# Kernel optimization log

Measured on AMD Instinct MI355X. Metric: run time of the kernel, lower is better.

The kernel has to match this reference:

```python
import jax, jax.numpy as jnp
import numpy as np
import math

D_MODEL = 1024
D_STATE = 16
D_CONV = 4
EXPAND = 2
D_INNER = EXPAND * D_MODEL
DT_RANK = 64
BATCH = 4
SEQ_LEN = 2048


def setup_inputs() -> dict:
    key = jax.random.key(0)
    ks = jax.random.split(key, 10)
    hidden_states = jax.random.normal(ks[0], (BATCH, SEQ_LEN, D_MODEL), jnp.float32)
    in_proj_w = jax.random.normal(ks[1], (D_MODEL, 2 * D_INNER), jnp.float32) * (D_MODEL ** -0.5)
    conv_w = jax.random.normal(ks[2], (D_INNER, D_CONV), jnp.float32) * (D_CONV ** -0.5)
    conv_b = jnp.zeros((D_INNER,), jnp.float32)
    x_proj_w = jax.random.normal(ks[3], (D_INNER, DT_RANK + 2 * D_STATE), jnp.float32) * (D_INNER ** -0.5)
    dt_init_std = DT_RANK ** -0.5
    dt_proj_w = jax.random.uniform(ks[4], (DT_RANK, D_INNER), jnp.float32, -dt_init_std, dt_init_std)
    # inverse-softplus init of dt bias: dt ~ logUniform(dt_min, dt_max)
    dt_min, dt_max, dt_floor = 0.001, 0.1, 1e-4
    dt = jnp.exp(jax.random.uniform(ks[5], (D_INNER,), jnp.float32) * (math.log(dt_max) - math.log(dt_min)) + math.log(dt_min))
    dt = jnp.clip(dt, dt_floor, None)
    dt_proj_b = dt + jnp.log(-jnp.expm1(-dt))
    A = jnp.tile(jnp.arange(1, D_STATE + 1, dtype=jnp.float32)[None, :], (D_INNER, 1))
    A_log = jnp.log(A)
    D = jnp.ones((D_INNER,), jnp.float32)
    out_proj_w = jax.random.normal(ks[6], (D_INNER, D_MODEL), jnp.float32) * (D_INNER ** -0.5)
    return {
        "hidden_states": hidden_states,
        "in_proj_w": in_proj_w,
        "conv_w": conv_w,
        "conv_b": conv_b,
        "x_proj_w": x_proj_w,
        "dt_proj_w": dt_proj_w,
        "dt_proj_b": dt_proj_b,
        "A_log": A_log,
        "D": D,
        "out_proj_w": out_proj_w,
    }


def _mamba_forward(hidden_states, in_proj_w, conv_w, conv_b, x_proj_w, dt_proj_w, dt_proj_b, A_log, D, out_proj_w):
    b, L, _ = hidden_states.shape
    d_state = A_log.shape[1]
    dt_rank = dt_proj_w.shape[0]
    K = conv_w.shape[1]

    xz = hidden_states @ in_proj_w                     # (b, L, 2*d_inner)
    x, z = jnp.split(xz, 2, axis=-1)                   # each (b, L, d_inner)

    # causal depthwise conv1d (padding = K-1, truncated to L)
    x_pad = jnp.pad(x, ((0, 0), (K - 1, 0), (0, 0)))
    x = sum(x_pad[:, k:k + L, :] * conv_w[:, k] for k in range(K)) + conv_b
    x = jax.nn.silu(x)

    x_dbl = x @ x_proj_w                               # (b, L, dt_rank + 2*d_state)
    dt, B, C = jnp.split(x_dbl, [dt_rank, dt_rank + d_state], axis=-1)
    dt = jax.nn.softplus(dt @ dt_proj_w + dt_proj_b)   # (b, L, d_inner)
    A = -jnp.exp(A_log)                                # (d_inner, d_state)

    def step(h, inp):
        x_t, dt_t, B_t, C_t = inp                      # (b,d), (b,d), (b,n), (b,n)
        dA = jnp.exp(A[None] * dt_t[..., None])        # (b, d, n)
        h = dA * h + dt_t[..., None] * B_t[:, None, :] * x_t[..., None]
        y_t = jnp.einsum('bdn,bn->bd', h, C_t) + D * x_t
        return h, y_t

    h0 = jnp.zeros((b, x.shape[-1], d_state), x.dtype)
    xs = (x.transpose(1, 0, 2), dt.transpose(1, 0, 2), B.transpose(1, 0, 2), C.transpose(1, 0, 2))
    _, ys = jax.lax.scan(step, h0, xs)                 # ys: (L, b, d_inner)
    y = ys.transpose(1, 0, 2) * jax.nn.silu(z)
    return y @ out_proj_w                              # (b, L, d_model)


def reference(hidden_states, in_proj_w, conv_w, conv_b, x_proj_w, dt_proj_w, dt_proj_b, A_log, D, out_proj_w):
    return _mamba_forward(hidden_states, in_proj_w, conv_w, conv_b, x_proj_w, dt_proj_w, dt_proj_b, A_log, D, out_proj_w)
```

## Files before the change

### kernel.cpp

```cpp
#include <hip/hip_runtime.h>
#include <hip/hip_bf16.h>


#define DM 1024
#define DS 16
#define DC 4
#define DI 2048
#define DR 64
#define NB 4
#define SL 2048
#define NTOK (NB*SL)
#define XDBL_W (DR + 2*DS)
#define CONV_R 8

typedef __hip_bfloat16 bf16;
typedef unsigned short u16;
typedef __attribute__((ext_vector_type(8))) short s8v;
typedef __attribute__((ext_vector_type(4))) float f4v;
typedef __attribute__((ext_vector_type(4))) unsigned short us4;

__device__ __forceinline__ float b2f(bf16 v) { return __bfloat162float(v); }
__device__ __forceinline__ bf16  f2b(float v) { return __float2bfloat16(v); }
__device__ __forceinline__ u16 f2u(float x) {
    union { bf16 h; u16 s; } u; u.h = f2b(x); return u.s;
}
__device__ __forceinline__ float u2f(u16 s) {
    union { bf16 h; u16 s; } u; u.s = s; return b2f(u.h);
}

__device__ __forceinline__ bool sniff_bf16(const void* Dones) {
    return ((const u16*)Dones)[0] == 0x3F80u;
}

__device__ __forceinline__ float softplus_fast(float v) {
    return fmaxf(v, 0.f) + __logf(1.f + __expf(-fabsf(v)));
}

template<int MODE>
__device__ __forceinline__ float ld(const void* p, size_t i, bool bf) {
    if (MODE == 0) return b2f(((const bf16*)p)[i]);
    if (MODE == 1) return ((const float*)p)[i];
    return bf ? b2f(((const bf16*)p)[i]) : ((const float*)p)[i];
}
template<int MODE>
__device__ __forceinline__ void st(void* p, size_t i, bool bf, float v) {
    if (MODE == 0)      { ((bf16*)p)[i] = f2b(v); }
    else if (MODE == 1) { ((float*)p)[i] = v; }
    else { if (bf) ((bf16*)p)[i] = f2b(v); else ((float*)p)[i] = v; }
}

template<int CM>
__device__ __forceinline__ void cstore(void* C, void* C2, size_t m, int n,
                                       int ldc, bool bf, float v) {
    if (CM == 3) {
        if (n < DR) ((bf16*)C2)[m * DR + n] = f2b(v);
        else        ((float*)C)[m * (2 * DS) + (n - DR)] = v;
    } else {
        st<CM>(C, m * (size_t)ldc + n, bf, v);
    }
}

#define AS1 __attribute__((address_space(1)))
#define AS3 __attribute__((address_space(3)))
__device__ __forceinline__ void gload_lds16(const void* g, void* l) {
    __builtin_amdgcn_global_load_lds((const AS1 unsigned int*)g,
                                     (AS3 unsigned int*)l, 16, 0, 0);
}

__global__ __launch_bounds__(256) void cast_bf16_kernel(
    const void* __restrict__ src, bf16* __restrict__ dst,
    const void* __restrict__ sniff)
{
    const bool bf = sniff_bf16(sniff);
    const size_t i = ((size_t)blockIdx.x * 256 + threadIdx.x) * 4;
    if (bf) {
        *(us4*)((u16*)dst + i) = *(const us4*)((const u16*)src + i);
    } else {
        const f4v f = *(const f4v*)((const float*)src + i);
        us4 o; o.x = f2u(f.x); o.y = f2u(f.y); o.z = f2u(f.z); o.w = f2u(f.w);
        *(us4*)((u16*)dst + i) = o;
    }
}

__global__ __launch_bounds__(256) void transpose_w(
    const void* __restrict__ w, bf16* __restrict__ wt,
    int K, int N, const void* __restrict__ sniff)
{
    const bool bf = sniff_bf16(sniff);
    __shared__ float t[32][33];
    const int tx = threadIdx.x & 31, ty = threadIdx.x >> 5;
    const int n0 = blockIdx.x * 32, k0 = blockIdx.y * 32;
    #pragma unroll
    for (int i = 0; i < 4; i++) {
        int k = k0 + ty + i * 8, n = n0 + tx;
        t[ty + i * 8][tx] = (n < N) ? ld<2>(w, (size_t)k * N + n, bf) : 0.f;
    }
    __syncthreads();
    #pragma unroll
    for (int i = 0; i < 4; i++) {
        int n = n0 + ty + i * 8, k = k0 + tx;
        wt[(size_t)n * K + k] = f2b(t[tx][ty + i * 8]);
    }
}

template<int BM, int BN, int WM, int WN, int CM>
__global__ __launch_bounds__(WM*WN*64, 2) void gemm_big(
    const bf16* __restrict__ A, int lda,
    const bf16* __restrict__ Bt,
    void* __restrict__ C, int ldc, int K,
    const void* __restrict__ sniff)
{
    constexpr int NT  = WM * WN;
    constexpr int NTH = NT * 64;
    constexpr int WAVE_M = BM / WM, WAVE_N = BN / WN;
    constexpr int MR = WAVE_M / 16, NR = WAVE_N / 16, MR2 = MR / 2;
    constexpr int CH_ROWS = NTH / 8;
    constexpr int ACH = BM / CH_ROWS;
    constexpr int BCH = BN / CH_ROWS;

    const bool bf = sniff_bf16(sniff);
    __shared__ short Asm[2][BM * 64];
    __shared__ short Bsm[2][BN * 64];

    const int tid = threadIdx.x, lane = tid & 63, wave = tid >> 6;
    const int wm = wave / WN, wn = wave % WN;
    const int ll = lane & 15, qd = lane >> 4;
    const int m0 = blockIdx.x * BM, n0 = blockIdx.y * BN;

    const int s_r  = tid >> 3;
    const int s_cb = ((tid & 7) * 16) ^ ((s_r & 7) << 4);

    const char* Ab = (const char*)A;
    const char* Bb = (const char*)Bt;

    f4v acc[MR][NR];
    #pragma unroll
    for (int i = 0; i < MR; i++)
        #pragma unroll
        for (int j = 0; j < NR; j++) acc[i][j] = (f4v){0.f, 0.f, 0.f, 0.f};

    #pragma unroll
    for (int c = 0; c < ACH; c++)
        gload_lds16(Ab + (((size_t)(m0 + c * CH_ROWS + s_r) * lda) << 1) + s_cb,
                    (char*)&Asm[0][0] + (c * NTH + tid) * 16);
    #pragma unroll
    for (int c = 0; c < BCH; c++)
        gload_lds16(Bb + (((size_t)(n0 + c * CH_ROWS + s_r) * K) << 1) + s_cb,
                    (char*)&Bsm[0][0] + (c * NTH + tid) * 16);
    asm volatile("s_waitcnt vmcnt(0)" ::: "memory");
    __builtin_amdgcn_sched_barrier(0);
    __builtin_amdgcn_s_barrier();

    const int NTILE = K >> 6;
    for (int t = 0; t < NTILE; ++t) {
        const int cur = t & 1, nxt = cur ^ 1;
        const int kk = (t + 1) << 6;
        const bool more = (t + 1 < NTILE);
        const char* Ac = (const char*)&Asm[cur][0];
        const char* Bc = (const char*)&Bsm[cur][0];
        #pragma unroll
        for (int p = 0; p < 4; ++p) {
            const int kh = p >> 1, mh = p & 1;
            const int kb = kh * 64;
            s8v af[MR2], bv[NR];
            #pragma unroll
            for (int i = 0; i < MR2; i++) {
                const int row = wm * WAVE_M + (mh * MR2 + i) * 16 + ll;
                af[i] = *(const s8v*)(Ac + (size_t)row * 128
                                        + ((kb + qd * 16) ^ ((ll & 7) << 4)));
            }
            #pragma unroll
            for (int j = 0; j < NR; j++) {
                const int row = wn * WAVE_N + j * 16 + ll;
                bv[j] = *(const s8v*)(Bc + (size_t)row * 128
                                        + ((kb + qd * 16) ^ ((ll & 7) << 4)));
            }
            if (p == 0 && more) {
                #pragma unroll
                for (int c = 0; c < ACH; c++)
                    gload_lds16(Ab + (((size_t)(m0 + c * CH_ROWS + s_r) * lda + kk) << 1) + s_cb,
                                (char*)&Asm[nxt][0] + (c * NTH + tid) * 16);
            }
            if (p == 1 && more) {
                #pragma unroll
                for (int c = 0; c < BCH; c++)
                    gload_lds16(Bb + (((size_t)(n0 + c * CH_ROWS + s_r) * K + kk) << 1) + s_cb,
                                (char*)&Bsm[nxt][0] + (c * NTH + tid) * 16);
            }
            __builtin_amdgcn_sched_barrier(0);
            __builtin_amdgcn_s_barrier();
            asm volatile("s_waitcnt lgkmcnt(0)" ::: "memory");
            __builtin_amdgcn_sched_barrier(0);
            __builtin_amdgcn_s_setprio(1);
            #pragma unroll
            for (int i = 0; i < MR2; i++)
                #pragma unroll
                for (int j = 0; j < NR; j++)
                    acc[mh * MR2 + i][j] = __builtin_amdgcn_mfma_f32_16x16x32_bf16(
                        af[i], bv[j], acc[mh * MR2 + i][j], 0, 0, 0);
            __builtin_amdgcn_s_setprio(0);
            if (p == 3) {
                asm volatile("s_waitcnt vmcnt(0)" ::: "memory");
            }
            __builtin_amdgcn_sched_barrier(0);
            __builtin_amdgcn_s_barrier();
        }
    }

    #pragma unroll
    for (int i = 0; i < MR; i++) {
        #pragma unroll
        for (int j = 0; j < NR; j++) {
            const int col = n0 + wn * WAVE_N + j * 16 + ll;
            #pragma unroll
            for (int r = 0; r < 4; r++) {
                const int row = m0 + wm * WAVE_M + i * 16 + qd * 4 + r;
                st<CM>(C, (size_t)row * ldc + col, bf, acc[i][j][r]);
            }
        }
    }
}

template<int CM, int EPI>
__global__ __launch_bounds__(256) void gemm_mfma(
    const bf16* __restrict__ A, int lda,
    const bf16* __restrict__ Bt,
    void* __restrict__ C, void* __restrict__ C2, int ldc,
    int M, int N, int K,
    const void* __restrict__ bias,
    const void* __restrict__ sniff)
{
    const bool bf = sniff_bf16(sniff);
    __shared__ short As[128 * 32];
    __shared__ short Bs[128 * 32];

    const int tid  = threadIdx.x;
    const int lane = tid & 63;
    const int wave = tid >> 6;
    const int wm = (wave & 1) * 64;
    const int wn = (wave >> 1) * 64;
    const int m0 = blockIdx.x * 128;
    const int n0 = blockIdx.y * 128;
    const int ll = lane & 15;
    const int qd = lane >> 4;

    const int srow  = lane >> 2;
    const int skoff = (lane & 3) * 8;

    const short* Ag = (const short*)A;
    const short* Bg = (const short*)Bt;
    char* AsB = (char*)As + wave * 2048 + lane * 16;
    char* BsB = (char*)Bs + wave * 2048 + lane * 16;
    const size_t a_row = (size_t)(m0 + wave * 32 + srow);
    const size_t b_row = (size_t)(n0 + wave * 32 + srow);

    f4v acc[4][4];
    #pragma unroll
    for (int i = 0; i < 4; i++)
        #pragma unroll
        for (int j = 0; j < 4; j++)
            acc[i][j] = (f4v){0.f, 0.f, 0.f, 0.f};

    for (int k0 = 0; k0 < K; k0 += 32) {
        gload_lds16(Ag + a_row * lda + k0 + skoff,            AsB);
        gload_lds16(Ag + (a_row + 16) * lda + k0 + skoff,     AsB + 1024);
        gload_lds16(Bg + b_row * K + k0 + skoff,              BsB);
        gload_lds16(Bg + (b_row + 16) * K + k0 + skoff,       BsB + 1024);
        __syncthreads();

        s8v af[4], bfr[4];
        #pragma unroll
        for (int s = 0; s < 4; s++)
            af[s] = *(const s8v*)&As[(wm + s * 16 + ll) * 32 + qd * 8];
        #pragma unroll
        for (int s = 0; s < 4; s++)
            bfr[s] = *(const s8v*)&Bs[(wn + s * 16 + ll) * 32 + qd * 8];
        #pragma unroll
        for (int i = 0; i < 4; i++)
            #pragma unroll
            for (int j = 0; j < 4; j++)
                acc[i][j] = __builtin_amdgcn_mfma_f32_16x16x32_bf16(
                    af[i], bfr[j], acc[i][j], 0, 0, 0);
        __syncthreads();
    }

    #pragma unroll
    for (int sn = 0; sn < 4; sn++) {
        const int cn = n0 + wn + sn * 16 + ll;
        if (cn >= N) continue;
        float bvv = 0.f;
        if (EPI == 1) bvv = ld<2>(bias, cn, bf);
        #pragma unroll
        for (int sm = 0; sm < 4; sm++) {
            #pragma unroll
            for (int r = 0; r < 4; r++) {
                const int cm = m0 + wm + sm * 16 + qd * 4 + r;
                float v = acc[sm][sn][r];
                if (EPI == 1) v = softplus_fast(v + bvv);
                cstore<CM>(C, C2, (size_t)cm, cn, ldc, bf, v);
            }
        }
    }
}

template<int AM, int CM, int EPI>
__global__ __launch_bounds__(256) void gemm_kernel(
    const void* __restrict__ A, int lda,
    const void* __restrict__ B, size_t bbase, int ldb,
    void* __restrict__ C, void* __restrict__ C2, int ldc,
    int M, int N, int K,
    const void* __restrict__ bias,
    const void* __restrict__ sniff)
{
    const bool bf = sniff_bf16(sniff);
    const int BM = 64, BN = 64, BK = 16;
    __shared__ float Asm[BK][BM + 4];
    __shared__ float Bsm[BK][BN + 4];

    const int tid = threadIdx.x;
    const int m0 = blockIdx.x * BM;
    const int n0 = blockIdx.y * BN;
    const int tx = tid % 16;
    const int ty = tid / 16;
    const int a_k = tid % BK;
    const int a_m = tid / BK;
    const int b_n = tid % BN;
    const int b_k = tid / BN;

    float acc[4][4] = {};

    for (int k0 = 0; k0 < K; k0 += BK) {
        #pragma unroll
        for (int i = 0; i < 4; i++) {
            int m = m0 + a_m + i * 16;
            float v = 0.f;
            if (m < M) v = ld<AM>(A, (size_t)m * lda + (k0 + a_k), bf);
            Asm[a_k][a_m + i * 16] = v;
        }
        #pragma unroll
        for (int i = 0; i < 4; i++) {
            int kk = b_k + i * 4;
            int n = n0 + b_n;
            float v = 0.f;
            if (n < N) v = ld<2>(B, bbase + (size_t)(k0 + kk) * ldb + n, bf);
            Bsm[kk][b_n] = v;
        }
        __syncthreads();
        #pragma unroll
        for (int kk = 0; kk < BK; kk++) {
            float av[4], bv[4];
            #pragma unroll
            for (int i = 0; i < 4; i++) av[i] = Asm[kk][ty * 4 + i];
            #pragma unroll
            for (int j = 0; j < 4; j++) bv[j] = Bsm[kk][tx * 4 + j];
            #pragma unroll
            for (int i = 0; i < 4; i++)
                #pragma unroll
                for (int j = 0; j < 4; j++)
                    acc[i][j] += av[i] * bv[j];
        }
        __syncthreads();
    }
    #pragma unroll
    for (int i = 0; i < 4; i++) {
        int m = m0 + ty * 4 + i;
        if (m >= M) continue;
        #pragma unroll
        for (int j = 0; j < 4; j++) {
            int n = n0 + tx * 4 + j;
            if (n >= N) continue;
            float v = acc[i][j];
            if (EPI == 1) {
                v += ld<2>(bias, n, bf);
                v = softplus_fast(v);
            }
            cstore<CM>(C, C2, (size_t)m, n, ldc, bf, v);
        }
    }
}

__global__ __launch_bounds__(256) void conv_silu_kernel(
    const bf16* __restrict__ xg, const void* __restrict__ w,
    const void* __restrict__ bias, bf16* __restrict__ xc,
    const void* __restrict__ sniff)
{
    const bool bf = sniff_bf16(sniff);
    const int c  = blockIdx.x * 256 + threadIdx.x;
    const int r0 = blockIdx.y * CONV_R;
    const int l0 = r0 % SL;

    float w0, w1, w2, w3;
    if (bf) {
        const us4 wv = *(const us4*)((const u16*)w + (size_t)c * 4);
        w0 = u2f(wv.x); w1 = u2f(wv.y); w2 = u2f(wv.z); w3 = u2f(wv.w);
    } else {
        const f4v wv = *(const f4v*)((const float*)w + (size_t)c * 4);
        w0 = wv.x; w1 = wv.y; w2 = wv.z; w3 = wv.w;
    }
    const float bs = ld<2>(bias, c, bf);

    float xm3 = (l0 >= 3) ? b2f(xg[(size_t)(r0 - 3) * DI + c]) : 0.f;
    float xm2 = (l0 >= 2) ? b2f(xg[(size_t)(r0 - 2) * DI + c]) : 0.f;
    float xm1 = (l0 >= 1) ? b2f(xg[(size_t)(r0 - 1) * DI + c]) : 0.f;

    #pragma unroll
    for (int i = 0; i < CONV_R; i++) {
        const size_t row = (size_t)(r0 + i);
        const float x0 = b2f(xg[row * DI + c]);
        const float acc = bs + w0 * xm3 + w1 * xm2 + w2 * xm1 + w3 * x0;
        const float s = acc / (1.f + __expf(-acc));
        xc[row * DI + c] = f2b(s);
        xm3 = xm2; xm2 = xm1; xm1 = x0;
    }
}

__global__ __launch_bounds__(256) void scan_pass1(
    const bf16* __restrict__ xc, const bf16* __restrict__ dt,
    const float* __restrict__ bc,
    const void* __restrict__ A_log, const void* __restrict__ Dones,
    float* __restrict__ P, float* __restrict__ Q, int nch)
{
    const bool bf = sniff_bf16(Dones);
    const int d = blockIdx.x * 256 + threadIdx.x;
    const int c = blockIdx.y;
    const int b = blockIdx.z;
    const int T = SL / nch;
    __shared__ float bcs[64 * 2 * DS];

    const size_t base = (size_t)b * SL + (size_t)c * T;
    for (int k = threadIdx.x; k < T * 2 * DS; k += 256)
        bcs[k] = bc[base * (2 * DS) + k];

    float a[DS], Qq[DS];
    bool lad = true;
    #pragma unroll
    for (int n = 0; n < DS; n++) {
        a[n] = -__expf(ld<2>(A_log, (size_t)d * DS + n, bf));
        Qq[n] = 0.f;
        lad = lad && (fabsf(a[n] - (n + 1) * a[0]) < 1e-3f);
    }
    __syncthreads();

    const u16* xp = (const u16*)xc + base * DI + d;
    const u16* tp = (const u16*)dt + base * DI + d;

    float Pp[DS];
    if (lad) {
        const float a0 = a[0];
        float R = 1.f;
        for (int i = 0; i < T; i++) {
            const float xv = u2f(xp[(size_t)i * DI]);
            const float tv = u2f(tp[(size_t)i * DI]);
            const float dtx = tv * xv;
            const float* Bv = &bcs[i * 2 * DS];
            const float r = __expf(a0 * tv);
            const float r2 = r * r, r3 = r2 * r, r4 = r2 * r2;
            float ca = r, cb = r2, cc = r3, cd = r4;
            R *= r;
            #pragma unroll
            for (int n = 0; n < DS; n += 4) {
                Qq[n]     = ca * Qq[n]     + dtx * Bv[n];
                Qq[n + 1] = cb * Qq[n + 1] + dtx * Bv[n + 1];
                Qq[n + 2] = cc * Qq[n + 2] + dtx * Bv[n + 2];
                Qq[n + 3] = cd * Qq[n + 3] + dtx * Bv[n + 3];
                ca *= r4; cb *= r4; cc *= r4; cd *= r4;
            }
        }
        const float R2 = R * R, R3 = R2 * R, R4 = R2 * R2;
        float pa = R, pb = R2, pc = R3, pd = R4;
        #pragma unroll
        for (int n = 0; n < DS; n += 4) {
            Pp[n] = pa; Pp[n + 1] = pb; Pp[n + 2] = pc; Pp[n + 3] = pd;
            pa *= R4; pb *= R4; pc *= R4; pd *= R4;
        }
    } else {
        #pragma unroll
        for (int n = 0; n < DS; n++) Pp[n] = 1.f;
        for (int i = 0; i < T; i++) {
            const float xv = u2f(xp[(size_t)i * DI]);
            const float tv = u2f(tp[(size_t)i * DI]);
            const float dtx = tv * xv;
            const float* Bv = &bcs[i * 2 * DS];
            #pragma unroll
            for (int n = 0; n < DS; n++) {
                const float dA = __expf(a[n] * tv);
                Pp[n] *= dA;
                Qq[n] = dA * Qq[n] + dtx * Bv[n];
            }
        }
    }
    const size_t ob = ((size_t)b * nch + c) * (DS * DI) + d;
    #pragma unroll
    for (int n = 0; n < DS; n++) {
        P[ob + (size_t)n * DI] = Pp[n];
        Q[ob + (size_t)n * DI] = Qq[n];
    }
}

__global__ __launch_bounds__(256) void scan_pass2(
    float* __restrict__ P, const float* __restrict__ Q, int nch)
{
    const int j = blockIdx.x * 256 + threadIdx.x;
    const int b = blockIdx.y;
    float h = 0.f;
    for (int c = 0; c < nch; c++) {
        const size_t o = ((size_t)b * nch + c) * (DI * DS) + j;
        const float p = P[o];
        const float q = Q[o];
        P[o] = h;
        h = p * h + q;
    }
}

__global__ __launch_bounds__(256) void scan_pass3(
    const bf16* __restrict__ xc, const bf16* __restrict__ dt,
    const float* __restrict__ bc, bf16* __restrict__ z,
    const void* __restrict__ A_log, const void* __restrict__ Dones,
    const float* __restrict__ H, int nch)
{
    const bool bf = sniff_bf16(Dones);
    const int d = blockIdx.x * 256 + threadIdx.x;
    const int c = blockIdx.y;
    const int b = blockIdx.z;
    const int T = SL / nch;
    __shared__ float bcs[64 * 2 * DS];

    const size_t base = (size_t)b * SL + (size_t)c * T;
    for (int k = threadIdx.x; k < T * 2 * DS; k += 256)
        bcs[k] = bc[base * (2 * DS) + k];

    float a[DS], h[DS];
    bool lad = true;
    const size_t ob = ((size_t)b * nch + c) * (DS * DI) + d;
    #pragma unroll
    for (int n = 0; n < DS; n++) {
        a[n] = -__expf(ld<2>(A_log, (size_t)d * DS + n, bf));
        h[n] = H[ob + (size_t)n * DI];
        lad = lad && (fabsf(a[n] - (n + 1) * a[0]) < 1e-3f);
    }
    const float dD = ld<2>(Dones, d, bf);
    __syncthreads();

    const u16* xp = (const u16*)xc + base * DI + d;
    const u16* tp = (const u16*)dt + base * DI + d;
    u16*       zp = (u16*)z + base * DI + d;

    if (lad) {
        const float a0 = a[0];
        for (int i = 0; i < T; i++) {
            const float xv = u2f(xp[(size_t)i * DI]);
            const float tv = u2f(tp[(size_t)i * DI]);
            const float zv = u2f(zp[(size_t)i * DI]);
            const float dtx = tv * xv;
            const float* Bv = &bcs[i * 2 * DS];
            const float* Cv = Bv + DS;
            const float r = __expf(a0 * tv);
            const float r2 = r * r, r3 = r2 * r, r4 = r2 * r2;
            float ca = r, cb = r2, cc = r3, cd = r4;
            float ya = dD * xv, yb = 0.f, yc = 0.f, yd = 0.f;
            #pragma unroll
            for (int n = 0; n < DS; n += 4) {
                h[n]     = ca * h[n]     + dtx * Bv[n];     ya += h[n]     * Cv[n];
                h[n + 1] = cb * h[n + 1] + dtx * Bv[n + 1]; yb += h[n + 1] * Cv[n + 1];
                h[n + 2] = cc * h[n + 2] + dtx * Bv[n + 2]; yc += h[n + 2] * Cv[n + 2];
                h[n + 3] = cd * h[n + 3] + dtx * Bv[n + 3]; yd += h[n + 3] * Cv[n + 3];
                ca *= r4; cb *= r4; cc *= r4; cd *= r4;
            }
            const float y = (ya + yb) + (yc + yd);
            const float g = zv / (1.f + __expf(-zv));
            zp[(size_t)i * DI] = f2u(y * g);
        }
    } else {
        for (int i = 0; i < T; i++) {
            const float xv = u2f(xp[(size_t)i * DI]);
            const float tv = u2f(tp[(size_t)i * DI]);
            const float zv = u2f(zp[(size_t)i * DI]);
            const float dtx = tv * xv;
            const float* Bv = &bcs[i * 2 * DS];
            const float* Cv = Bv + DS;
            float y = dD * xv;
            #pragma unroll
            for (int n = 0; n < DS; n++) {
                const float dA = __expf(a[n] * tv);
                h[n] = dA * h[n] + dtx * Bv[n];
                y += h[n] * Cv[n];
            }
            const float g = zv / (1.f + __expf(-zv));
            zp[(size_t)i * DI] = f2u(y * g);
        }
    }
}

__global__ __launch_bounds__(256) void scan_serial(
    const bf16* __restrict__ xc, const bf16* __restrict__ dt,
    const float* __restrict__ bc, bf16* __restrict__ z,
    const void* __restrict__ A_log, const void* __restrict__ Dones)
{
    const bool bf = sniff_bf16(Dones);
    const int d = blockIdx.x * 256 + threadIdx.x;
    const int b = blockIdx.y;
    float a[DS], h[DS];
    #pragma unroll
    for (int n = 0; n < DS; n++) {
        a[n] = -__expf(ld<2>(A_log, (size_t)d * DS + n, bf));
        h[n] = 0.f;
    }
    const float dD = ld<2>(Dones, d, bf);
    const size_t base = (size_t)b * SL;
    for (int l = 0; l < SL; l++) {
        const size_t row = base + l;
        const float xv  = b2f(xc[row * DI + d]);
        const float dtv = b2f(dt[row * DI + d]);
        const float* Bv = bc + row * (2 * DS);
        const float dtx = dtv * xv;
        float y = dD * xv;
        #pragma unroll
        for (int n = 0; n < DS; n++) {
            const float dA = __expf(a[n] * dtv);
            h[n] = dA * h[n] + dtx * Bv[n];
            y += h[n] * Bv[DS + n];
        }
        const float zv = b2f(z[row * DI + d]);
        const float g = zv / (1.f + __expf(-zv));
        z[row * DI + d] = f2b(y * g);
    }
}

extern "C" void kernel_launch(void* const* d_in, const int* in_sizes, int n_in,
                              void* d_out, int out_size, void* d_ws, size_t ws_size,
                              hipStream_t stream) {
    const void* hs        = d_in[0];
    const void* in_proj_w = d_in[1];
    const void* conv_w    = d_in[2];
    const void* conv_b    = d_in[3];
    const void* x_proj_w  = d_in[4];
    const void* dt_proj_w = d_in[5];
    const void* dt_proj_b = d_in[6];
    const void* A_log     = d_in[7];
    const void* Dones     = d_in[8];
    const void* out_proj_w= d_in[9];

    char* ws = (char*)d_ws;
    bf16*  xg   = (bf16*)(ws);
    bf16*  xc   = (bf16*)(ws + 33554432);
    bf16*  hsb  = (bf16*)(ws + 33554432);
    bf16*  z    = (bf16*)(ws + 67108864);
    float* bc   = (float*)(ws + 100663296);
    bf16*  dtf  = (bf16*)(ws + 101711872);
    const size_t WT_OFF = 102760448;
    bf16* in_projT  = (bf16*)(ws + WT_OFF);
    bf16* x_projT   = (bf16*)(ws + WT_OFF);
    bf16* dt_projT  = (bf16*)(ws + WT_OFF + 524288);
    bf16* out_projT = (bf16*)(ws + WT_OFF);
    const bool mfma_ok = ws_size >= WT_OFF + 8388608;

    const size_t per_chunk = (size_t)NB * DI * DS * 4 * 2;
    int nch = 32;
    while (nch > 1 && WT_OFF + (size_t)nch * per_chunk > ws_size) nch >>= 1;
    const bool chunked = (WT_OFF + (size_t)nch * per_chunk <= ws_size);
    float* P = (float*)(ws + WT_OFF);
    float* Q = P + (size_t)NB * nch * DI * DS;

    bf16* dtb = xg;

    if (mfma_ok) {
        cast_bf16_kernel<<<(NTOK*DM/4)/256, 256, 0, stream>>>(hs, hsb, Dones);
        transpose_w<<<dim3((2*DI)/32, DM/32), 256, 0, stream>>>(
            in_proj_w, in_projT, DM, 2*DI, Dones);
        gemm_big<256, 256, 2, 4, 0><<<dim3(NTOK/256, DI/256), 512, 0, stream>>>(
            hsb, DM, in_projT, xg, DI, DM, Dones);
        gemm_big<256, 256, 2, 4, 0><<<dim3(NTOK/256, DI/256), 512, 0, stream>>>(
            hsb, DM, in_projT + (size_t)DI * DM, z, DI, DM, Dones);
        conv_silu_kernel<<<dim3(DI/256, NTOK/CONV_R), 256, 0, stream>>>(
            xg, conv_w, conv_b, xc, Dones);
        transpose_w<<<dim3(128/32, DI/32), 256, 0, stream>>>(
            x_proj_w, x_projT, DI, XDBL_W, Dones);
        gemm_mfma<3, 0><<<dim3(NTOK/128, 1), 256, 0, stream>>>(
            xc, DI, x_projT, bc, dtf, 0, NTOK, XDBL_W, DI, nullptr, Dones);
        transpose_w<<<dim3(DI/32, DR/32), 256, 0, stream>>>(
            dt_proj_w, dt_projT, DR, DI, Dones);
        gemm_mfma<0, 1><<<dim3(NTOK/128, DI/128), 256, 0, stream>>>(
            dtf, DR, dt_projT, dtb, nullptr, DI, NTOK, DI, DR, dt_proj_b, Dones);
    } else {
        gemm_kernel<2, 0, 0><<<dim3(NTOK/64, DI/64), 256, 0, stream>>>(
            hs, DM, in_proj_w, 0, 2*DI, xg, nullptr, DI, NTOK, DI, DM, nullptr, Dones);
        gemm_kernel<2, 0, 0><<<dim3(NTOK/64, DI/64), 256, 0, stream>>>(
            hs, DM, in_proj_w, DI, 2*DI, z, nullptr, DI, NTOK, DI, DM, nullptr, Dones);
        conv_silu_kernel<<<dim3(DI/256, NTOK/CONV_R), 256, 0, stream>>>(
            xg, conv_w, conv_b, xc, Dones);
        gemm_kernel<0, 3, 0><<<dim3(NTOK/64, (XDBL_W + 63)/64), 256, 0, stream>>>(
            xc, DI, x_proj_w, 0, XDBL_W, bc, dtf, 0, NTOK, XDBL_W, DI, nullptr, Dones);
        gemm_kernel<0, 0, 1><<<dim3(NTOK/64, DI/64), 256, 0, stream>>>(
            dtf, DR, dt_proj_w, 0, DI, dtb, nullptr, DI, NTOK, DI, DR, dt_proj_b, Dones);
    }

    if (chunked) {
        scan_pass1<<<dim3(DI/256, nch, NB), 256, 0, stream>>>(
            xc, dtb, bc, A_log, Dones, P, Q, nch);
        scan_pass2<<<dim3((DI*DS)/256, NB), 256, 0, stream>>>(P, Q, nch);
        scan_pass3<<<dim3(DI/256, nch, NB), 256, 0, stream>>>(
            xc, dtb, bc, z, A_log, Dones, P, nch);
    } else {
        scan_serial<<<dim3(DI/256, NB), 256, 0, stream>>>(
            xc, dtb, bc, z, A_log, Dones);
    }

    if (mfma_ok) {
        transpose_w<<<dim3(DM/32, DI/32), 256, 0, stream>>>(
            out_proj_w, out_projT, DI, DM, Dones);
        gemm_big<256, 128, 4, 2, 2><<<dim3(NTOK/256, DM/128), 512, 0, stream>>>(
            z, DI, out_projT, d_out, DM, DI, Dones);
    } else {
        gemm_kernel<0, 2, 0><<<dim3(NTOK/64, DM/64), 256, 0, stream>>>(
            z, DI, out_proj_w, 0, DM, d_out, nullptr, DM, NTOK, DM, DI, nullptr, Dones);
    }
}
```

Before: 469.9 us.

## Vectorize scan recurrences with packed float2 math and raise chunk count to 64

```diff
diff --git a/kernel.cpp b/kernel.cpp
--- a/kernel.cpp
+++ b/kernel.cpp
@@ -17,6 +17,7 @@
 typedef unsigned short u16;
 typedef __attribute__((ext_vector_type(8))) short s8v;
 typedef __attribute__((ext_vector_type(4))) float f4v;
+typedef __attribute__((ext_vector_type(2))) float f2v;
 typedef __attribute__((ext_vector_type(4))) unsigned short us4;
 
 __device__ __forceinline__ float b2f(bf16 v) { return __bfloat162float(v); }
@@ -34,6 +35,10 @@
 
 __device__ __forceinline__ float softplus_fast(float v) {
     return fmaxf(v, 0.f) + __logf(1.f + __expf(-fabsf(v)));
+}
+
+__device__ __forceinline__ float silu_fast(float v) {
+    return v * __builtin_amdgcn_rcpf(1.f + __expf(-v));
 }
 
 template<int MODE>
@@ -431,12 +436,11 @@
     for (int k = threadIdx.x; k < T * 2 * DS; k += 256)
         bcs[k] = bc[base * (2 * DS) + k];
 
-    float a[DS], Qq[DS];
+    float a[DS];
     bool lad = true;
     #pragma unroll
     for (int n = 0; n < DS; n++) {
         a[n] = -__expf(ld<2>(A_log, (size_t)d * DS + n, bf));
-        Qq[n] = 0.f;
         lad = lad && (fabsf(a[n] - (n + 1) * a[0]) < 1e-3f);
     }
     __syncthreads();
@@ -444,26 +448,32 @@
     const u16* xp = (const u16*)xc + base * DI + d;
     const u16* tp = (const u16*)dt + base * DI + d;
 
-    float Pp[DS];
+    float Pp[DS], Qq[DS];
     if (lad) {
         const float a0 = a[0];
         float R = 1.f;
+        f2v q2[8];
+        #pragma unroll
+        for (int j = 0; j < 8; j++) q2[j] = (f2v){0.f, 0.f};
         for (int i = 0; i < T; i++) {
             const float xv = u2f(xp[(size_t)i * DI]);
             const float tv = u2f(tp[(size_t)i * DI]);
             const float dtx = tv * xv;
-            const float* Bv = &bcs[i * 2 * DS];
+            const f4v* B4 = (const f4v*)&bcs[i * 2 * DS];
             const float r = __expf(a0 * tv);
-            const float r2 = r * r, r3 = r2 * r, r4 = r2 * r2;
-            float ca = r, cb = r2, cc = r3, cd = r4;
+            const float r2 = r * r, r4 = r2 * r2;
+            const f2v r4v = {r4, r4};
+            f2v cA = {r, r2};
+            f2v cB = {r2 * r, r4};
+            const f2v dtx2 = {dtx, dtx};
             R *= r;
             #pragma unroll
-            for (int n = 0; n < DS; n += 4) {
-                Qq[n]     = ca * Qq[n]     + dtx * Bv[n];
-                Qq[n + 1] = cb * Qq[n + 1] + dtx * Bv[n + 1];
-                Qq[n + 2] = cc * Qq[n + 2] + dtx * Bv[n + 2];
-                Qq[n + 3] = cd * Qq[n + 3] + dtx * Bv[n + 3];
-                ca *= r4; cb *= r4; cc *= r4; cd *= r4;
+            for (int j4 = 0; j4 < 4; j4++) {
+                const f4v Bq = B4[j4];
+                const f2v b0 = {Bq.x, Bq.y}, b1 = {Bq.z, Bq.w};
+                q2[2 * j4]     = cA * q2[2 * j4]     + dtx2 * b0;
+                q2[2 * j4 + 1] = cB * q2[2 * j4 + 1] + dtx2 * b1;
+                cA *= r4v; cB *= r4v;
             }
         }
         const float R2 = R * R, R3 = R2 * R, R4 = R2 * R2;
@@ -473,9 +483,11 @@
             Pp[n] = pa; Pp[n + 1] = pb; Pp[n + 2] = pc; Pp[n + 3] = pd;
             pa *= R4; pb *= R4; pc *= R4; pd *= R4;
         }
+        #pragma unroll
+        for (int j = 0; j < 8; j++) { Qq[2 * j] = q2[j].x; Qq[2 * j + 1] = q2[j].y; }
     } else {
         #pragma unroll
-        for (int n = 0; n < DS; n++) Pp[n] = 1.f;
+        for (int n = 0; n < DS; n++) { Pp[n] = 1.f; Qq[n] = 0.f; }
         for (int i = 0; i < T; i++) {
             const float xv = u2f(xp[(size_t)i * DI]);
             const float tv = u2f(tp[(size_t)i * DI]);
@@ -529,13 +541,12 @@
     for (int k = threadIdx.x; k < T * 2 * DS; k += 256)
         bcs[k] = bc[base * (2 * DS) + k];
 
-    float a[DS], h[DS];
+    float a[DS];
     bool lad = true;
     const size_t ob = ((size_t)b * nch + c) * (DS * DI) + d;
     #pragma unroll
     for (int n = 0; n < DS; n++) {
         a[n] = -__expf(ld<2>(A_log, (size_t)d * DS + n, bf));
-        h[n] = H[ob + (size_t)n * DI];
         lad = lad && (fabsf(a[n] - (n + 1) * a[0]) < 1e-3f);
     }
     const float dD = ld<2>(Dones, d, bf);
@@ -547,30 +558,43 @@
 
     if (lad) {
         const float a0 = a[0];
+        f2v h2[8];
+        #pragma unroll
+        for (int j = 0; j < 8; j++)
+            h2[j] = (f2v){H[ob + (size_t)(2 * j) * DI],
+                          H[ob + (size_t)(2 * j + 1) * DI]};
         for (int i = 0; i < T; i++) {
             const float xv = u2f(xp[(size_t)i * DI]);
             const float tv = u2f(tp[(size_t)i * DI]);
             const float zv = u2f(zp[(size_t)i * DI]);
             const float dtx = tv * xv;
-            const float* Bv = &bcs[i * 2 * DS];
-            const float* Cv = Bv + DS;
+            const f4v* B4 = (const f4v*)&bcs[i * 2 * DS];
+            const f4v* C4 = B4 + 4;
             const float r = __expf(a0 * tv);
-            const float r2 = r * r, r3 = r2 * r, r4 = r2 * r2;
-            float ca = r, cb = r2, cc = r3, cd = r4;
-            float ya = dD * xv, yb = 0.f, yc = 0.f, yd = 0.f;
-            #pragma unroll
-            for (int n = 0; n < DS; n += 4) {
-                h[n]     = ca * h[n]     + dtx * Bv[n];     ya += h[n]     * Cv[n];
-                h[n + 1] = cb * h[n + 1] + dtx * Bv[n + 1]; yb += h[n + 1] * Cv[n + 1];
-                h[n + 2] = cc * h[n + 2] + dtx * Bv[n + 2]; yc += h[n + 2] * Cv[n + 2];
-                h[n + 3] = cd * h[n + 3] + dtx * Bv[n + 3]; yd += h[n + 3] * Cv[n + 3];
-                ca *= r4; cb *= r4; cc *= r4; cd *= r4;
-            }
-            const float y = (ya + yb) + (yc + yd);
-            const float g = zv / (1.f + __expf(-zv));
-            zp[(size_t)i * DI] = f2u(y * g);
+            const float r2 = r * r, r4 = r2 * r2;
+            const f2v r4v = {r4, r4};
+            f2v cA = {r, r2};
+            f2v cB = {r2 * r, r4};
+            const f2v dtx2 = {dtx, dtx};
+            f2v ya = {dD * xv, 0.f}, yb = {0.f, 0.f};
+            #pragma unroll
+            for (int j4 = 0; j4 < 4; j4++) {
+                const f4v Bq = B4[j4], Cq = C4[j4];
+                const f2v b0 = {Bq.x, Bq.y}, b1 = {Bq.z, Bq.w};
+                const f2v c0 = {Cq.x, Cq.y}, c1 = {Cq.z, Cq.w};
+                h2[2 * j4]     = cA * h2[2 * j4]     + dtx2 * b0;
+                ya += h2[2 * j4] * c0;
+                h2[2 * j4 + 1] = cB * h2[2 * j4 + 1] + dtx2 * b1;
+                yb += h2[2 * j4 + 1] * c1;
+                cA *= r4v; cB *= r4v;
+            }
+            const float y = (ya.x + ya.y) + (yb.x + yb.y);
+            zp[(size_t)i * DI] = f2u(y * silu_fast(zv));
         }
     } else {
+        float h[DS];
+        #pragma unroll
+        for (int n = 0; n < DS; n++) h[n] = H[ob + (size_t)n * DI];
         for (int i = 0; i < T; i++) {
             const float xv = u2f(xp[(size_t)i * DI]);
             const float tv = u2f(tp[(size_t)i * DI]);
@@ -585,8 +609,7 @@
                 h[n] = dA * h[n] + dtx * Bv[n];
                 y += h[n] * Cv[n];
             }
-            const float g = zv / (1.f + __expf(-zv));
-            zp[(size_t)i * DI] = f2u(y * g);
+            zp[(size_t)i * DI] = f2u(y * silu_fast(zv));
         }
     }
 }
@@ -655,9 +678,10 @@
     const bool mfma_ok = ws_size >= WT_OFF + 8388608;
 
     const size_t per_chunk = (size_t)NB * DI * DS * 4 * 2;
-    int nch = 32;
+    int nch = 64;
     while (nch > 1 && WT_OFF + (size_t)nch * per_chunk > ws_size) nch >>= 1;
-    const bool chunked = (WT_OFF + (size_t)nch * per_chunk <= ws_size);
+    const bool chunked = (nch >= 32) &&
+                         (WT_OFF + (size_t)nch * per_chunk <= ws_size);
     float* P = (float*)(ws + WT_OFF);
     float* Q = P + (size_t)NB * nch * DI * DS;
 
```

New measurement: 461.3 us. About the same (-1.8%).
